# Optimization experiments

Hardware: AMD Instinct MI355X
Metric: run time of the kernel (lower is better)

Reference implementation:

```python
import jax, jax.numpy as jnp
import numpy as np

B, S, HID, HEADS = 1, 2048, 4096, 32
HEAD_D = HID // HEADS
SCALE = float(1.0 / np.sqrt(HEAD_D))  # = 1/norm_factor^2 with use_mup=False


def setup_inputs() -> dict:
    key = jax.random.key(0)
    k0, k1, k2, k3, k4 = jax.random.split(key, 5)
    return {
        "x": jax.random.normal(k0, (B, S, HID), jnp.float32),
        "attn_qkvw": jax.random.normal(k1, (HID, 3 * HID), jnp.float32) * 0.02,
        "attn_qkvb": jax.random.normal(k2, (3 * HID,), jnp.float32) * 0.02,
        "attn_ow": jax.random.normal(k3, (HID, HID), jnp.float32) * 0.02,
        "attn_ob": jax.random.normal(k4, (HID,), jnp.float32) * 0.02,
    }


def reference(x, attn_qkvw, attn_qkvb, attn_ow, attn_ob):
    # QKV projection (LinearOp): [B,S,HID] @ [HID,3*HID] + bias -> packed qkv
    qkv = x @ attn_qkvw + attn_qkvb
    q, k, v = jnp.split(qkv, 3, axis=-1)  # each [B,S,HID]

    def to_heads(t):
        return t.reshape(B, S, HEADS, HEAD_D)

    q, k, v = to_heads(q), to_heads(k), to_heads(v)
    # flash kernel math: softmax(scale * q k^T + causal mask) @ v (numerically
    # stable online softmax == standard stable softmax)
    scores = jnp.einsum("bqhd,bkhd->bhqk", q, k) * jnp.float32(SCALE)
    causal = jnp.tril(jnp.ones((S, S), dtype=bool))  # P_SEQ = 0
    scores = jnp.where(causal[None, None], scores, jnp.float32(-jnp.inf))
    attn = jax.nn.softmax(scores, axis=-1)
    ctx = jnp.einsum("bhqk,bkhd->bqhd", attn, v).reshape(B, S, HID)
    # output projection
    return ctx @ attn_ow + attn_ob
```

## Files before the change

kernel.cpp:

```cpp
#include <hip/hip_runtime.h>
#include <hip/hip_bf16.h>
#include <math.h>

typedef __bf16 bf16_t;
typedef __bf16 bf16x8 __attribute__((ext_vector_type(8)));
typedef float f32x4 __attribute__((ext_vector_type(4)));

#define AS1 __attribute__((address_space(1)))
#define AS3 __attribute__((address_space(3)))

static constexpr int S_  = 2048;
static constexpr int HID = 4096;
static constexpr int NH  = 32;
static constexpr int HD  = 128;
static constexpr int N3  = 3 * HID;
static constexpr float SCALE = 0.08838834764831845f;

__global__ void cvt_f32_bf16(const float* __restrict__ in, bf16_t* __restrict__ out, int n4) {
  int i = blockIdx.x * blockDim.x + threadIdx.x;
  if (i >= n4) return;
  float4 v = ((const float4*)in)[i];
  union { bf16_t h[4]; short4 s4; } u;
  u.h[0] = (bf16_t)v.x; u.h[1] = (bf16_t)v.y; u.h[2] = (bf16_t)v.z; u.h[3] = (bf16_t)v.w;
  ((short4*)out)[i] = u.s4;
}

__global__ void transcvt(const float* __restrict__ in, bf16_t* __restrict__ out, int R, int C) {
  __shared__ float t[32][33];
  int r0 = blockIdx.y * 32, c0 = blockIdx.x * 32;
  int tx = threadIdx.x, ty = threadIdx.y;
#pragma unroll
  for (int i = 0; i < 32; i += 8)
    t[ty + i][tx] = in[(size_t)(r0 + ty + i) * C + c0 + tx];
  __syncthreads();
#pragma unroll
  for (int i = 0; i < 32; i += 8)
    out[(size_t)(c0 + ty + i) * R + r0 + tx] = (bf16_t)t[tx][ty + i];
}

__global__ void vtrans(const bf16_t* __restrict__ qkv, bf16_t* __restrict__ vt) {
  __shared__ bf16_t t[32][33];
  int h = blockIdx.z;
  int s0 = blockIdx.x * 32, d0 = blockIdx.y * 32;
  int tx = threadIdx.x, ty = threadIdx.y;
#pragma unroll
  for (int i = 0; i < 32; i += 8)
    t[ty + i][tx] = qkv[(size_t)(s0 + ty + i) * N3 + 2 * HID + h * HD + d0 + tx];
  __syncthreads();
#pragma unroll
  for (int i = 0; i < 32; i += 8)
    vt[(size_t)(h * HD + d0 + ty + i) * S_ + s0 + tx] = t[tx][ty + i];
}


template <bool STG, int VMC>
__device__ __forceinline__ void tile_step(
    char* __restrict__ smem, int slotbase, int aoff, int boff,
    const bf16_t* gA, const bf16_t* gB, int kst, size_t sk128,
    char* stg_dst, f32x4 (&acc)[8][4]) {
  const char* ab = smem + slotbase;
  const char* bb = smem + slotbase + 16384;
  bf16x8 a[4], b[4];
#pragma unroll
  for (int ni = 0; ni < 4; ++ni) b[ni] = *(const bf16x8*)(bb + boff + ni * 1024);
#pragma unroll
  for (int mi = 0; mi < 4; ++mi) a[mi] = *(const bf16x8*)(ab + aoff + mi * 1024);
  if constexpr (STG) {
    __builtin_amdgcn_global_load_lds((const AS1 void*)(gA + kst), (AS3 void*)(stg_dst), 16, 0, 0);
    __builtin_amdgcn_global_load_lds((const AS1 void*)(gA + sk128 + kst), (AS3 void*)(stg_dst + 8192), 16, 0, 0);
  }
  __builtin_amdgcn_s_barrier();
  __builtin_amdgcn_s_setprio(1);
#pragma unroll
  for (int mi = 0; mi < 4; ++mi)
#pragma unroll
    for (int ni = 0; ni < 4; ++ni)
      acc[mi][ni] = __builtin_amdgcn_mfma_f32_16x16x32_bf16(a[mi], b[ni], acc[mi][ni], 0, 0, 0);
  __builtin_amdgcn_s_setprio(0);
  __builtin_amdgcn_s_barrier();
#pragma unroll
  for (int mi = 0; mi < 4; ++mi) a[mi] = *(const bf16x8*)(ab + aoff + (4 + mi) * 1024);
  if constexpr (STG) {
    __builtin_amdgcn_global_load_lds((const AS1 void*)(gB + kst), (AS3 void*)(stg_dst + 16384), 16, 0, 0);
    __builtin_amdgcn_global_load_lds((const AS1 void*)(gB + sk128 + kst), (AS3 void*)(stg_dst + 24576), 16, 0, 0);
  }
  if constexpr (VMC == 8)      asm volatile("s_waitcnt vmcnt(8)" ::: "memory");
  else if constexpr (VMC == 4) asm volatile("s_waitcnt vmcnt(4)" ::: "memory");
  else if constexpr (VMC == 0) asm volatile("s_waitcnt vmcnt(0)" ::: "memory");
  __builtin_amdgcn_s_barrier();
  __builtin_amdgcn_s_setprio(1);
#pragma unroll
  for (int mi = 0; mi < 4; ++mi)
#pragma unroll
    for (int ni = 0; ni < 4; ++ni)
      acc[4 + mi][ni] = __builtin_amdgcn_mfma_f32_16x16x32_bf16(a[mi], b[ni], acc[4 + mi][ni], 0, 0, 0);
  __builtin_amdgcn_s_setprio(0);
  __builtin_amdgcn_s_barrier();
}

template <typename OutT>
__global__ __launch_bounds__(512, 2) void gemm256(
    const bf16_t* __restrict__ A, const bf16_t* __restrict__ BT,
    const float* __restrict__ bias, OutT* __restrict__ C,
    int M, int N, int K) {
  extern __shared__ char smem[];
  const int tid = threadIdx.x;
  const int wv = tid >> 6, ln = tid & 63;
  const int lr = ln & 15, lg = ln >> 4;
  const int wm = wv >> 2, wn = wv & 3;

  const int nx = N >> 8;
  const int qx = gridDim.x >> 3;
  const int wg = (blockIdx.x & 7) * qx + (blockIdx.x >> 3);
  const int m0 = (wg / nx) * 256, n0 = (wg % nx) * 256;

  const int lrow = wv * 16 + (ln >> 2);
  const int lcol = ((ln & 3) << 3) ^ ((ln & 32) >> 1);
  const bf16_t* gA = A + (size_t)(m0 + lrow) * K + lcol;
  const bf16_t* gB = BT + (size_t)(n0 + lrow) * K + lcol;
  const size_t sk128 = (size_t)128 * K;
  char* stg_wbase = smem + wv * 1024;

  const int sw = (lr & 8) << 2;
  const int aoff = (wm * 128 + lr) * 64 + ((lg * 16) ^ sw);
  const int boff = (wn * 64 + lr) * 64 + ((lg * 16) ^ sw);

  f32x4 acc[8][4] = {};

#pragma unroll
  for (int t = 0; t < 3; ++t) {
    char* d = stg_wbase + t * 32768;
    __builtin_amdgcn_global_load_lds((const AS1 void*)(gA + t * 32), (AS3 void*)(d), 16, 0, 0);
    __builtin_amdgcn_global_load_lds((const AS1 void*)(gA + sk128 + t * 32), (AS3 void*)(d + 8192), 16, 0, 0);
    __builtin_amdgcn_global_load_lds((const AS1 void*)(gB + t * 32), (AS3 void*)(d + 16384), 16, 0, 0);
    __builtin_amdgcn_global_load_lds((const AS1 void*)(gB + sk128 + t * 32), (AS3 void*)(d + 24576), 16, 0, 0);
  }
  asm volatile("s_waitcnt vmcnt(8)" ::: "memory");
  __builtin_amdgcn_s_barrier();

  const int NT = K >> 5;
  int t = 0;
  for (; t < NT - 3; ++t)
    tile_step<true, 8>(smem, (t & 3) * 32768, aoff, boff, gA, gB, (t + 3) * 32,
                       sk128, stg_wbase + ((t + 3) & 3) * 32768, acc);
  tile_step<false, 4>(smem, (t & 3) * 32768, aoff, boff, gA, gB, 0, sk128, smem, acc); ++t;
  tile_step<false, 0>(smem, (t & 3) * 32768, aoff, boff, gA, gB, 0, sk128, smem, acc); ++t;
  tile_step<false, -1>(smem, (t & 3) * 32768, aoff, boff, gA, gB, 0, sk128, smem, acc);

#pragma unroll
  for (int mi = 0; mi < 8; ++mi)
#pragma unroll
    for (int ni = 0; ni < 4; ++ni) {
      const int col = n0 + wn * 64 + ni * 16 + lr;
      const float bv = bias[col];
#pragma unroll
      for (int i = 0; i < 4; ++i) {
        const int row = m0 + wm * 128 + mi * 16 + lg * 4 + i;
        C[(size_t)row * N + col] = (OutT)(acc[mi][ni][i] + bv);
      }
    }
}

__global__ __launch_bounds__(256, 4) void attn_fwd(
    const bf16_t* __restrict__ qkv, const bf16_t* __restrict__ vt,
    bf16_t* __restrict__ ctx) {
  __shared__ __align__(16) bf16_t Ks[64][136];
  __shared__ __align__(16) bf16_t Vts[128][72];

  const int tid = threadIdx.x;
  const int wv = tid >> 6, ln = tid & 63;
  bf16_t* Pl = &Ks[0][0] + wv * (16 * 72);

  const int bid = blockIdx.x;
  const int h  = ((bid & 7) << 2) + (bid >> 8);
  const int qt = 31 - ((((bid >> 3) & 31) + ((bid >> 8) << 3)) & 31);
  const int q0 = qt * 64;
  const int lr = ln & 15, lg = ln >> 4;

  bf16x8 qf[4];
#pragma unroll
  for (int kk = 0; kk < 4; ++kk) {
    bf16x8 r = *(const bf16x8*)(qkv + (size_t)(q0 + 16 * wv + lr) * N3 + h * HD + kk * 32 + lg * 8);
#pragma unroll
    for (int j = 0; j < 8; ++j) r[j] = (bf16_t)((float)r[j] * SCALE);
    qf[kk] = r;
  }

  f32x4 oacc[8] = {};
  float mrow[4], psum[4];
#pragma unroll
  for (int i = 0; i < 4; ++i) { mrow[i] = -INFINITY; psum[i] = 0.f; }

  const int ntiles = qt + 1;
  for (int t = 0; t < ntiles; ++t) {
    const int kv0 = t * 64;
    __syncthreads();
#pragma unroll
    for (int it = 0; it < 4; ++it) {
      int c = tid + it * 256;
      {
        int row = c >> 4, col = (c & 15) * 8;
        *(bf16x8*)&Ks[row][col] =
            *(const bf16x8*)(qkv + (size_t)(kv0 + row) * N3 + HID + h * HD + col);
      }
      {
        int row = c >> 3, col = (c & 7) * 8;
        *(bf16x8*)&Vts[row][col] =
            *(const bf16x8*)(vt + (size_t)(h * HD + row) * S_ + kv0 + col);
      }
    }
    __syncthreads();

    f32x4 sacc[4] = {};
#pragma unroll
    for (int kk = 0; kk < 4; ++kk)
#pragma unroll
      for (int ni = 0; ni < 4; ++ni) {
        bf16x8 kf = *(const bf16x8*)&Ks[16 * ni + lr][kk * 32 + lg * 8];
        sacc[ni] = __builtin_amdgcn_mfma_f32_16x16x32_bf16(qf[kk], kf, sacc[ni], 0, 0, 0);
      }

    const bool needmask = (kv0 + 63 > q0 + 16 * wv);
    float p[4][4];
    float mx[4];
    bool grow = false;
#pragma unroll
    for (int i = 0; i < 4; ++i) {
      const int row = q0 + 16 * wv + lg * 4 + i;
      float m_ = -INFINITY;
#pragma unroll
      for (int ni = 0; ni < 4; ++ni) {
        float s = sacc[ni][i];
        if (needmask && (kv0 + 16 * ni + lr > row)) s = -INFINITY;
        p[ni][i] = s;
        m_ = fmaxf(m_, s);
      }
      m_ = fmaxf(m_, __shfl_xor(m_, 1, 64));
      m_ = fmaxf(m_, __shfl_xor(m_, 2, 64));
      m_ = fmaxf(m_, __shfl_xor(m_, 4, 64));
      m_ = fmaxf(m_, __shfl_xor(m_, 8, 64));
      mx[i] = m_;
      grow |= (m_ > mrow[i]);
    }
    if (__any(grow)) {
      float alpha[4];
#pragma unroll
      for (int i = 0; i < 4; ++i) {
        const float mn = fmaxf(mrow[i], mx[i]);
        alpha[i] = __expf(mrow[i] - mn);
        mrow[i] = mn;
        psum[i] *= alpha[i];
      }
#pragma unroll
      for (int nf = 0; nf < 8; ++nf)
#pragma unroll
        for (int i = 0; i < 4; ++i) oacc[nf][i] *= alpha[i];
    }
#pragma unroll
    for (int i = 0; i < 4; ++i) {
      float ps = 0.f;
#pragma unroll
      for (int ni = 0; ni < 4; ++ni) {
        float e = __expf(p[ni][i] - mrow[i]);
        p[ni][i] = e;
        ps += e;
      }
      psum[i] += ps;
    }

    __syncthreads();

#pragma unroll
    for (int ni = 0; ni < 4; ++ni)
#pragma unroll
      for (int i = 0; i < 4; ++i)
        Pl[(lg * 4 + i) * 72 + 16 * ni + lr] = (bf16_t)p[ni][i];

#pragma unroll
    for (int kk2 = 0; kk2 < 2; ++kk2) {
      bf16x8 pf = *(const bf16x8*)&Pl[lr * 72 + kk2 * 32 + lg * 8];
#pragma unroll
      for (int nf = 0; nf < 8; ++nf) {
        bf16x8 vf = *(const bf16x8*)&Vts[16 * nf + lr][kk2 * 32 + lg * 8];
        oacc[nf] = __builtin_amdgcn_mfma_f32_16x16x32_bf16(pf, vf, oacc[nf], 0, 0, 0);
      }
    }
  }

#pragma unroll
  for (int i = 0; i < 4; ++i) {
    float s = psum[i];
    s += __shfl_xor(s, 1, 64);
    s += __shfl_xor(s, 2, 64);
    s += __shfl_xor(s, 4, 64);
    s += __shfl_xor(s, 8, 64);
    psum[i] = 1.f / s;
  }
#pragma unroll
  for (int nf = 0; nf < 8; ++nf)
#pragma unroll
    for (int i = 0; i < 4; ++i) {
      int row = q0 + 16 * wv + lg * 4 + i;
      int col = h * HD + 16 * nf + lr;
      ctx[(size_t)row * HID + col] = (bf16_t)(oacc[nf][i] * psum[i]);
    }
}

extern "C" void kernel_launch(void* const* d_in, const int* in_sizes, int n_in,
                              void* d_out, int out_size, void* d_ws, size_t ws_size,
                              hipStream_t stream) {
  const float* x    = (const float*)d_in[0];
  const float* wqkv = (const float*)d_in[1];
  const float* bqkv = (const float*)d_in[2];
  const float* ow   = (const float*)d_in[3];
  const float* ob   = (const float*)d_in[4];
  float* out = (float*)d_out;

  char* w = (char*)d_ws;
  bf16_t* xb    = (bf16_t*)(w);
  bf16_t* wqkvT = (bf16_t*)(w + (size_t)16777216);
  bf16_t* qkv   = (bf16_t*)(w + (size_t)117440512);
  bf16_t* vt    = (bf16_t*)(w + (size_t)167772160);
  bf16_t* ctx   = (bf16_t*)(w + (size_t)184549376);
  bf16_t* owT   = (bf16_t*)(w + (size_t)201326592);

  (void)in_sizes; (void)n_in; (void)out_size; (void)ws_size;

  cvt_f32_bf16<<<(S_ * HID / 4 + 255) / 256, 256, 0, stream>>>(x, xb, S_ * HID / 4);
  transcvt<<<dim3(N3 / 32, HID / 32), dim3(32, 8), 0, stream>>>(wqkv, wqkvT, HID, N3);
  transcvt<<<dim3(HID / 32, HID / 32), dim3(32, 8), 0, stream>>>(ow, owT, HID, HID);
  gemm256<bf16_t><<<(S_ / 256) * (N3 / 256), 512, 131072, stream>>>(xb, wqkvT, bqkv, qkv, S_, N3, HID);
  vtrans<<<dim3(S_ / 32, HD / 32, NH), dim3(32, 8), 0, stream>>>(qkv, vt);
  attn_fwd<<<(S_ / 64) * NH, 256, 0, stream>>>(qkv, vt, ctx);
  gemm256<float><<<(S_ / 256) * (HID / 256), 512, 131072, stream>>>(ctx, owT, ob, out, S_, HID, HID);
}
```

Baseline: 585.0 us.

## Shrink GEMM tiles to 256x128 with 3-slot LDS pipeline for more blocks

Replaces the 256x256 GEMM tile with a 256x128 tile. Each wave now computes 64x64 instead of 128x64, the LDS ring drops from four 32KB slots to three 24KB slots (72KB total), and launch bounds ask for 4 blocks per CU. The grid doubles, which improves load balance across CUs: the out-projection goes from 128 to 256 blocks and QKV from 384 to 768. The cost is lower arithmetic intensity per tile, more global and L2 traffic, and a shallower prefetch depth of two tiles ahead instead of three.

```diff
diff --git a/kernel.cpp b/kernel.cpp
--- a/kernel.cpp
+++ b/kernel.cpp
@@ -55,20 +55,21 @@
 
 template <bool STG, int VMC>
 __device__ __forceinline__ void tile_step(
-    char* __restrict__ smem, int slotbase, int aoff, int boff,
-    const bf16_t* gA, const bf16_t* gB, int kst, size_t sk128,
-    char* stg_dst, f32x4 (&acc)[8][4]) {
-  const char* ab = smem + slotbase;
-  const char* bb = smem + slotbase + 16384;
+    const char* slot, int aoff, int boff,
+    const bf16_t* gA, const bf16_t* gB, int kst, size_t skA,
+    char* stg_dst, f32x4 (&acc)[4][4]) {
   bf16x8 a[4], b[4];
 #pragma unroll
-  for (int ni = 0; ni < 4; ++ni) b[ni] = *(const bf16x8*)(bb + boff + ni * 1024);
-#pragma unroll
-  for (int mi = 0; mi < 4; ++mi) a[mi] = *(const bf16x8*)(ab + aoff + mi * 1024);
+  for (int mi = 0; mi < 4; ++mi) a[mi] = *(const bf16x8*)(slot + aoff + mi * 1024);
+#pragma unroll
+  for (int ni = 0; ni < 4; ++ni) b[ni] = *(const bf16x8*)(slot + 16384 + boff + ni * 1024);
   if constexpr (STG) {
     __builtin_amdgcn_global_load_lds((const AS1 void*)(gA + kst), (AS3 void*)(stg_dst), 16, 0, 0);
-    __builtin_amdgcn_global_load_lds((const AS1 void*)(gA + sk128 + kst), (AS3 void*)(stg_dst + 8192), 16, 0, 0);
-  }
+    __builtin_amdgcn_global_load_lds((const AS1 void*)(gA + skA + kst), (AS3 void*)(stg_dst + 8192), 16, 0, 0);
+    __builtin_amdgcn_global_load_lds((const AS1 void*)(gB + kst), (AS3 void*)(stg_dst + 16384), 16, 0, 0);
+  }
+  if constexpr (VMC == 3) asm volatile("s_waitcnt vmcnt(3)" ::: "memory");
+  else if constexpr (VMC == 0) asm volatile("s_waitcnt vmcnt(0)" ::: "memory");
   __builtin_amdgcn_s_barrier();
   __builtin_amdgcn_s_setprio(1);
 #pragma unroll
@@ -78,28 +79,10 @@
       acc[mi][ni] = __builtin_amdgcn_mfma_f32_16x16x32_bf16(a[mi], b[ni], acc[mi][ni], 0, 0, 0);
   __builtin_amdgcn_s_setprio(0);
   __builtin_amdgcn_s_barrier();
-#pragma unroll
-  for (int mi = 0; mi < 4; ++mi) a[mi] = *(const bf16x8*)(ab + aoff + (4 + mi) * 1024);
-  if constexpr (STG) {
-    __builtin_amdgcn_global_load_lds((const AS1 void*)(gB + kst), (AS3 void*)(stg_dst + 16384), 16, 0, 0);
-    __builtin_amdgcn_global_load_lds((const AS1 void*)(gB + sk128 + kst), (AS3 void*)(stg_dst + 24576), 16, 0, 0);
-  }
-  if constexpr (VMC == 8)      asm volatile("s_waitcnt vmcnt(8)" ::: "memory");
-  else if constexpr (VMC == 4) asm volatile("s_waitcnt vmcnt(4)" ::: "memory");
-  else if constexpr (VMC == 0) asm volatile("s_waitcnt vmcnt(0)" ::: "memory");
-  __builtin_amdgcn_s_barrier();
-  __builtin_amdgcn_s_setprio(1);
-#pragma unroll
-  for (int mi = 0; mi < 4; ++mi)
-#pragma unroll
-    for (int ni = 0; ni < 4; ++ni)
-      acc[4 + mi][ni] = __builtin_amdgcn_mfma_f32_16x16x32_bf16(a[mi], b[ni], acc[4 + mi][ni], 0, 0, 0);
-  __builtin_amdgcn_s_setprio(0);
-  __builtin_amdgcn_s_barrier();
 }
 
 template <typename OutT>
-__global__ __launch_bounds__(512, 2) void gemm256(
+__global__ __launch_bounds__(512, 4) void gemm_p(
     const bf16_t* __restrict__ A, const bf16_t* __restrict__ BT,
     const float* __restrict__ bias, OutT* __restrict__ C,
     int M, int N, int K) {
@@ -107,55 +90,57 @@
   const int tid = threadIdx.x;
   const int wv = tid >> 6, ln = tid & 63;
   const int lr = ln & 15, lg = ln >> 4;
-  const int wm = wv >> 2, wn = wv & 3;
-
-  const int nx = N >> 8;
+  const int wm = wv >> 1, wn = wv & 1;
+
+  const int nx = N >> 7;
   const int qx = gridDim.x >> 3;
   const int wg = (blockIdx.x & 7) * qx + (blockIdx.x >> 3);
-  const int m0 = (wg / nx) * 256, n0 = (wg % nx) * 256;
+  const int m0 = (wg / nx) * 256, n0 = (wg % nx) * 128;
 
   const int lrow = wv * 16 + (ln >> 2);
   const int lcol = ((ln & 3) << 3) ^ ((ln & 32) >> 1);
   const bf16_t* gA = A + (size_t)(m0 + lrow) * K + lcol;
   const bf16_t* gB = BT + (size_t)(n0 + lrow) * K + lcol;
-  const size_t sk128 = (size_t)128 * K;
-  char* stg_wbase = smem + wv * 1024;
+  const size_t skA = (size_t)128 * K;
 
   const int sw = (lr & 8) << 2;
-  const int aoff = (wm * 128 + lr) * 64 + ((lg * 16) ^ sw);
+  const int aoff = (wm * 64 + lr) * 64 + ((lg * 16) ^ sw);
   const int boff = (wn * 64 + lr) * 64 + ((lg * 16) ^ sw);
 
-  f32x4 acc[8][4] = {};
-
-#pragma unroll
-  for (int t = 0; t < 3; ++t) {
-    char* d = stg_wbase + t * 32768;
+  f32x4 acc[4][4] = {};
+
+#pragma unroll
+  for (int t = 0; t < 2; ++t) {
+    char* d = smem + t * 24576 + wv * 1024;
     __builtin_amdgcn_global_load_lds((const AS1 void*)(gA + t * 32), (AS3 void*)(d), 16, 0, 0);
-    __builtin_amdgcn_global_load_lds((const AS1 void*)(gA + sk128 + t * 32), (AS3 void*)(d + 8192), 16, 0, 0);
+    __builtin_amdgcn_global_load_lds((const AS1 void*)(gA + skA + t * 32), (AS3 void*)(d + 8192), 16, 0, 0);
     __builtin_amdgcn_global_load_lds((const AS1 void*)(gB + t * 32), (AS3 void*)(d + 16384), 16, 0, 0);
-    __builtin_amdgcn_global_load_lds((const AS1 void*)(gB + sk128 + t * 32), (AS3 void*)(d + 24576), 16, 0, 0);
-  }
-  asm volatile("s_waitcnt vmcnt(8)" ::: "memory");
+  }
+  asm volatile("s_waitcnt vmcnt(3)" ::: "memory");
   __builtin_amdgcn_s_barrier();
 
   const int NT = K >> 5;
+  int slot = 0, nslot = 2;
   int t = 0;
-  for (; t < NT - 3; ++t)
-    tile_step<true, 8>(smem, (t & 3) * 32768, aoff, boff, gA, gB, (t + 3) * 32,
-                       sk128, stg_wbase + ((t + 3) & 3) * 32768, acc);
-  tile_step<false, 4>(smem, (t & 3) * 32768, aoff, boff, gA, gB, 0, sk128, smem, acc); ++t;
-  tile_step<false, 0>(smem, (t & 3) * 32768, aoff, boff, gA, gB, 0, sk128, smem, acc); ++t;
-  tile_step<false, -1>(smem, (t & 3) * 32768, aoff, boff, gA, gB, 0, sk128, smem, acc);
-
-#pragma unroll
-  for (int mi = 0; mi < 8; ++mi)
+  for (; t < NT - 2; ++t) {
+    tile_step<true, 3>(smem + slot * 24576, aoff, boff, gA, gB, (t + 2) * 32,
+                       skA, smem + nslot * 24576 + wv * 1024, acc);
+    slot = (slot == 2) ? 0 : slot + 1;
+    nslot = (nslot == 2) ? 0 : nslot + 1;
+  }
+  tile_step<false, 0>(smem + slot * 24576, aoff, boff, gA, gB, 0, skA, smem, acc);
+  slot = (slot == 2) ? 0 : slot + 1;
+  tile_step<false, -1>(smem + slot * 24576, aoff, boff, gA, gB, 0, skA, smem, acc);
+
+#pragma unroll
+  for (int mi = 0; mi < 4; ++mi)
 #pragma unroll
     for (int ni = 0; ni < 4; ++ni) {
       const int col = n0 + wn * 64 + ni * 16 + lr;
       const float bv = bias[col];
 #pragma unroll
       for (int i = 0; i < 4; ++i) {
-        const int row = m0 + wm * 128 + mi * 16 + lg * 4 + i;
+        const int row = m0 + wm * 64 + mi * 16 + lg * 4 + i;
         C[(size_t)row * N + col] = (OutT)(acc[mi][ni][i] + bv);
       }
     }
@@ -329,8 +314,8 @@
   cvt_f32_bf16<<<(S_ * HID / 4 + 255) / 256, 256, 0, stream>>>(x, xb, S_ * HID / 4);
   transcvt<<<dim3(N3 / 32, HID / 32), dim3(32, 8), 0, stream>>>(wqkv, wqkvT, HID, N3);
   transcvt<<<dim3(HID / 32, HID / 32), dim3(32, 8), 0, stream>>>(ow, owT, HID, HID);
-  gemm256<bf16_t><<<(S_ / 256) * (N3 / 256), 512, 131072, stream>>>(xb, wqkvT, bqkv, qkv, S_, N3, HID);
+  gemm_p<bf16_t><<<(S_ / 256) * (N3 / 128), 512, 73728, stream>>>(xb, wqkvT, bqkv, qkv, S_, N3, HID);
   vtrans<<<dim3(S_ / 32, HD / 32, NH), dim3(32, 8), 0, stream>>>(qkv, vt);
   attn_fwd<<<(S_ / 64) * NH, 256, 0, stream>>>(qkv, vt, ctx);
-  gemm256<float><<<(S_ / 256) * (HID / 256), 512, 131072, stream>>>(ctx, owT, ob, out, S_, HID, HID);
-}
+  gemm_p<float><<<(S_ / 256) * (HID / 128), 512, 73728, stream>>>(ctx, owT, ob, out, S_, HID, HID);
+}
```

Result: faster. 550.6 us (-5.9%).
